# Kernel tuning notes

Hardware: AMD Instinct MI355X
Metric: run time of the kernel (lower is better)

## Reference

```python
import jax, jax.numpy as jnp
import numpy as np

B, T, D, U, W = 8, 1024, 1024, 1024, 2  # batch, seq_len, input_dim, units, window_size


def setup_inputs() -> dict:
    key = jax.random.key(0)
    k1, k2 = jax.random.split(key)
    x = jax.random.normal(k1, (B, T, D), dtype=jnp.float32)
    # keras 'uniform' initializer: U(-0.05, 0.05); kernel squeezed from (W,1,D,3U) to (W,D,3U)
    kernel = jax.random.uniform(k2, (W, D, 3 * U), dtype=jnp.float32, minval=-0.05, maxval=0.05)
    bias = jnp.zeros((3 * U,), dtype=jnp.float32)  # 'zero' initializer
    return {"x": x, "kernel": kernel, "bias": bias}


def reference(x, kernel, bias):
    Wk, Din, U3 = kernel.shape
    Un = U3 // 3
    Tn = x.shape[1]
    # causal temporal padding (window_size-1 on the left), then valid windowed conv
    xp = jnp.pad(x, ((0, 0), (Wk - 1, 0), (0, 0)))
    # gates[b,t] = sum_k xp[b,t+k] @ kernel[k] + bias  -> [B,T,3U]
    gates = sum(jnp.einsum('btd,du->btu', xp[:, k:k + Tn], kernel[k]) for k in range(Wk)) + bias
    z = jnp.tanh(gates[..., :Un])
    f = jax.nn.sigmoid(gates[..., Un:2 * Un])
    o = jax.nn.sigmoid(gates[..., 2 * Un:])

    def step(h, zfo):
        zt, ft, ot = zfo
        h_new = ot * (ft * h + (1.0 - ft) * zt)
        return h_new, h_new

    h0 = jnp.zeros((x.shape[0], Un), dtype=x.dtype)
    _, hs = jax.lax.scan(step, h0, (z.swapaxes(0, 1), f.swapaxes(0, 1), o.swapaxes(0, 1)))
    return hs.swapaxes(0, 1)  # [B,T,U] (return_sequences=True)
```

## Files before the change

### kernel.cpp

```cpp
#include <hip/hip_runtime.h>
#include <hip/hip_bf16.h>

typedef __bf16 bf16x8 __attribute__((ext_vector_type(8)));
typedef float f32x4 __attribute__((ext_vector_type(4)));

#define GLOBAL_AS(p) ((const __attribute__((address_space(1))) void*)(p))
#define LDS_AS(p)    ((__attribute__((address_space(3))) void*)(p))

static __device__ __forceinline__ unsigned short f2bf(float f) {
    union { float f; unsigned u; } v; v.f = f;
    unsigned r = v.u + 0x7FFFu + ((v.u >> 16) & 1u);
    return (unsigned short)(r >> 16);
}

__global__ void zero_page(float4* __restrict__ z) {
    z[threadIdx.x * 4 + 0] = make_float4(0.f, 0.f, 0.f, 0.f);
    z[threadIdx.x * 4 + 1] = make_float4(0.f, 0.f, 0.f, 0.f);
    z[threadIdx.x * 4 + 2] = make_float4(0.f, 0.f, 0.f, 0.f);
    z[threadIdx.x * 4 + 3] = make_float4(0.f, 0.f, 0.f, 0.f);
}

__global__ void prep_xb(const float* __restrict__ x, unsigned short* __restrict__ xb) {
    const int m = blockIdx.x;
    const int c = threadIdx.x * 4;
    float4 v = *reinterpret_cast<const float4*>(x + (size_t)m * 1024 + c);
    ushort4 b = make_ushort4(f2bf(v.x), f2bf(v.y), f2bf(v.z), f2bf(v.w));
    *reinterpret_cast<ushort4*>(xb + (size_t)m * 1024 + c) = b;
}

__global__ void prep_kt(const float* __restrict__ K, unsigned short* __restrict__ KT) {
    __shared__ float tile[64][65];
    const int bi = blockIdx.x;
    const int bj = blockIdx.y;
    const int tx = threadIdx.x & 63;
    const int ty = threadIdx.x >> 6;

#pragma unroll
    for (int i = 0; i < 16; ++i) {
        int r = ty * 16 + i;
        tile[r][tx] = K[(size_t)(bi * 64 + r) * 3072 + bj * 64 + tx];
    }
    __syncthreads();
#pragma unroll
    for (int i = 0; i < 16; ++i) {
        int r = ty * 16 + i;
        KT[(size_t)(bj * 64 + r) * 2048 + bi * 64 + tx] = f2bf(tile[tx][r]);
    }
}

__global__ __launch_bounds__(256, 2)
void gemm_gates(const unsigned short* __restrict__ xb,
                const unsigned short* __restrict__ BT,
                const unsigned short* __restrict__ zpage,
                const float* __restrict__ bias,
                float* __restrict__ G) {
    __shared__ __align__(16) unsigned short As[128 * 64];
    __shared__ __align__(16) unsigned short Bs[128 * 64];

    const int tid  = threadIdx.x;
    const int lane = tid & 63;
    const int wid  = tid >> 6;
    const int wr   = wid >> 1, wc = wid & 1;
    const int m0   = blockIdx.y * 128;
    const int n0   = blockIdx.x * 128;

    f32x4 acc[4][4] = {};

    const int sr = lane >> 3;
    const int sc = lane & 7;

    const unsigned short* srcA_lo[4];
    const unsigned short* srcA_hi[4];
    const unsigned short* srcB[4];
#pragma unroll
    for (int i = 0; i < 4; ++i) {
        const int r  = wid * 32 + i * 8 + sr;
        const int cc = sc ^ (r & 7);
        const int srow = m0 + r;
        srcA_hi[i] = xb + (size_t)srow * 1024 + cc * 8;
        srcA_lo[i] = ((srow & 1023) == 0) ? (zpage + cc * 8)
                                          : (xb + (size_t)(srow - 1) * 1024 + cc * 8);
        srcB[i]    = BT + (size_t)(n0 + r) * 2048 + cc * 8;
    }

    for (int kt = 0; kt < 32; ++kt) {
        const int kb = kt * 64;
#pragma unroll
        for (int i = 0; i < 4; ++i) {
            const int r0 = wid * 32 + i * 8;
            const unsigned short* sa = (kt < 16) ? (srcA_lo[i] + kb)
                                                 : (srcA_hi[i] + (kb - 1024));
            __builtin_amdgcn_global_load_lds(GLOBAL_AS(sa),          LDS_AS(As + r0 * 64), 16, 0, 0);
            __builtin_amdgcn_global_load_lds(GLOBAL_AS(srcB[i] + kb), LDS_AS(Bs + r0 * 64), 16, 0, 0);
        }
        __syncthreads();

#pragma unroll
        for (int ks = 0; ks < 2; ++ks) {
            bf16x8 af[4], bg[4];
#pragma unroll
            for (int m = 0; m < 4; ++m) {
                const int row = wr * 64 + m * 16 + (lane & 15);
                const int c   = ks * 4 + (lane >> 4);
                const int p   = c ^ (row & 7);
                af[m] = *reinterpret_cast<const bf16x8*>(As + row * 64 + p * 8);
            }
#pragma unroll
            for (int n = 0; n < 4; ++n) {
                const int row = wc * 64 + n * 16 + (lane & 15);
                const int c   = ks * 4 + (lane >> 4);
                const int p   = c ^ (row & 7);
                bg[n] = *reinterpret_cast<const bf16x8*>(Bs + row * 64 + p * 8);
            }
#pragma unroll
            for (int m = 0; m < 4; ++m)
#pragma unroll
                for (int n = 0; n < 4; ++n)
                    acc[m][n] = __builtin_amdgcn_mfma_f32_16x16x32_bf16(af[m], bg[n], acc[m][n], 0, 0, 0);
        }
        __syncthreads();
    }

    const int rgn = n0 >> 10;
#pragma unroll
    for (int m = 0; m < 4; ++m) {
#pragma unroll
        for (int n = 0; n < 4; ++n) {
            const int col = n0 + wc * 64 + n * 16 + (lane & 15);
            const float bv = bias[col];
#pragma unroll
            for (int v = 0; v < 4; ++v) {
                const int row = m0 + wr * 64 + m * 16 + ((lane >> 4) * 4) + v;
                const float g = acc[m][n][v] + bv;
                float val;
                if (rgn == 0) {
                    float s = 1.0f / (1.0f + __expf(-2.0f * g));
                    val = 2.0f * s - 1.0f;
                } else {
                    val = 1.0f / (1.0f + __expf(-g));
                }
                G[(size_t)row * 3072 + col] = val;
            }
        }
    }
}

__global__ void scan_pass1(const float* __restrict__ G, float2* __restrict__ AB) {
    const int bid = blockIdx.x;
    const int ug  = bid & 3;
    const int c   = (bid >> 2) & 7;
    const int b   = bid >> 5;
    const int u   = ug * 256 + threadIdx.x;
    const float* g = G + (size_t)(b * 1024 + c * 128) * 3072 + u;
    float A = 1.f, Bv = 0.f;
#pragma unroll 8
    for (int i = 0; i < 128; ++i) {
        const float zv = g[(size_t)i * 3072];
        const float fv = g[(size_t)i * 3072 + 1024];
        const float ov = g[(size_t)i * 3072 + 2048];
        const float a  = ov * fv;
        const float bb = ov * (1.f - fv) * zv;
        A  = a * A;
        Bv = a * Bv + bb;
    }
    AB[(size_t)(b * 8 + c) * 1024 + u] = make_float2(A, Bv);
}

__global__ void scan_pass23(const float* __restrict__ G, const float2* __restrict__ AB,
                            float* __restrict__ out) {
    const int b  = blockIdx.x >> 3;
    const int ug = blockIdx.x & 7;
    const int c  = threadIdx.x >> 7;
    const int ui = threadIdx.x & 127;
    const int u  = ug * 128 + ui;

    float h = 0.f;
    for (int j = 0; j < c; ++j) {
        float2 p = AB[(size_t)(b * 8 + j) * 1024 + u];
        h = p.x * h + p.y;
    }
    const float* g = G + (size_t)(b * 1024 + c * 128) * 3072 + u;
    float* o = out + (size_t)(b * 1024 + c * 128) * 1024 + u;
#pragma unroll 8
    for (int i = 0; i < 128; ++i) {
        const float zv = g[(size_t)i * 3072];
        const float fv = g[(size_t)i * 3072 + 1024];
        const float ov = g[(size_t)i * 3072 + 2048];
        h = ov * (fv * h + (1.f - fv) * zv);
        o[(size_t)i * 1024] = h;
    }
}

extern "C" void kernel_launch(void* const* d_in, const int* in_sizes, int n_in,
                              void* d_out, int out_size, void* d_ws, size_t ws_size,
                              hipStream_t stream) {
    const float* x    = (const float*)d_in[0];
    const float* kern = (const float*)d_in[1];
    const float* bias = (const float*)d_in[2];
    float* out = (float*)d_out;

    char* ws = (char*)d_ws;
    unsigned short* xb   = (unsigned short*)ws;
    unsigned short* KT   = (unsigned short*)(ws + 16777216);
    float* G             = (float*)(ws + 29360128);
    float2* AB           = (float2*)(ws + 130023424);
    unsigned short* zpg  = (unsigned short*)(ws + 130547712);

    zero_page<<<1, 64, 0, stream>>>((float4*)zpg);
    prep_xb<<<dim3(8192), dim3(256), 0, stream>>>(x, xb);
    prep_kt<<<dim3(32, 48), dim3(256), 0, stream>>>(kern, KT);
    gemm_gates<<<dim3(24, 64), dim3(256), 0, stream>>>(xb, KT, zpg, bias, G);
    scan_pass1<<<dim3(256), dim3(256), 0, stream>>>(G, AB);
    scan_pass23<<<dim3(64), dim3(1024), 0, stream>>>(G, AB, out);
}
```

Measured before the change: 177.6 us.

## Rewrite gate GEMM as 256x256 double-buffered pipeline with padded input and fp16 gates

```diff
diff --git a/kernel.cpp b/kernel.cpp
--- a/kernel.cpp
+++ b/kernel.cpp
@@ -13,19 +13,18 @@
     return (unsigned short)(r >> 16);
 }
 
-__global__ void zero_page(float4* __restrict__ z) {
-    z[threadIdx.x * 4 + 0] = make_float4(0.f, 0.f, 0.f, 0.f);
-    z[threadIdx.x * 4 + 1] = make_float4(0.f, 0.f, 0.f, 0.f);
-    z[threadIdx.x * 4 + 2] = make_float4(0.f, 0.f, 0.f, 0.f);
-    z[threadIdx.x * 4 + 3] = make_float4(0.f, 0.f, 0.f, 0.f);
-}
-
-__global__ void prep_xb(const float* __restrict__ x, unsigned short* __restrict__ xb) {
-    const int m = blockIdx.x;
+__global__ void prep_xb(const float* __restrict__ x, unsigned short* __restrict__ xb2) {
+    const int bid = blockIdx.x;
     const int c = threadIdx.x * 4;
-    float4 v = *reinterpret_cast<const float4*>(x + (size_t)m * 1024 + c);
-    ushort4 b = make_ushort4(f2bf(v.x), f2bf(v.y), f2bf(v.z), f2bf(v.w));
-    *reinterpret_cast<ushort4*>(xb + (size_t)m * 1024 + c) = b;
+    if (bid < 8192) {
+        const int dst = bid + (bid >> 10) + 1;
+        float4 v = *reinterpret_cast<const float4*>(x + (size_t)bid * 1024 + c);
+        ushort4 b = make_ushort4(f2bf(v.x), f2bf(v.y), f2bf(v.z), f2bf(v.w));
+        *reinterpret_cast<ushort4*>(xb2 + (size_t)dst * 1024 + c) = b;
+    } else {
+        const int zr = (bid - 8192) * 1025;
+        *reinterpret_cast<ushort4*>(xb2 + (size_t)zr * 1024 + c) = make_ushort4(0, 0, 0, 0);
+    }
 }
 
 __global__ void prep_kt(const float* __restrict__ K, unsigned short* __restrict__ KT) {
@@ -48,90 +47,145 @@
     }
 }
 
-__global__ __launch_bounds__(256, 2)
-void gemm_gates(const unsigned short* __restrict__ xb,
+__global__ __launch_bounds__(512, 2)
+void gemm_gates(const unsigned short* __restrict__ xb2,
                 const unsigned short* __restrict__ BT,
-                const unsigned short* __restrict__ zpage,
                 const float* __restrict__ bias,
-                float* __restrict__ G) {
-    __shared__ __align__(16) unsigned short As[128 * 64];
-    __shared__ __align__(16) unsigned short Bs[128 * 64];
+                _Float16* __restrict__ G) {
+    __shared__ __align__(16) unsigned short As[2 * 256 * 64];
+    __shared__ __align__(16) unsigned short Bs[2 * 256 * 64];
 
     const int tid  = threadIdx.x;
     const int lane = tid & 63;
-    const int wid  = tid >> 6;
-    const int wr   = wid >> 1, wc = wid & 1;
-    const int m0   = blockIdx.y * 128;
-    const int n0   = blockIdx.x * 128;
-
-    f32x4 acc[4][4] = {};
-
-    const int sr = lane >> 3;
-    const int sc = lane & 7;
-
-    const unsigned short* srcA_lo[4];
-    const unsigned short* srcA_hi[4];
-    const unsigned short* srcB[4];
-#pragma unroll
-    for (int i = 0; i < 4; ++i) {
-        const int r  = wid * 32 + i * 8 + sr;
-        const int cc = sc ^ (r & 7);
-        const int srow = m0 + r;
-        srcA_hi[i] = xb + (size_t)srow * 1024 + cc * 8;
-        srcA_lo[i] = ((srow & 1023) == 0) ? (zpage + cc * 8)
-                                          : (xb + (size_t)(srow - 1) * 1024 + cc * 8);
-        srcB[i]    = BT + (size_t)(n0 + r) * 2048 + cc * 8;
-    }
-
-    for (int kt = 0; kt < 32; ++kt) {
-        const int kb = kt * 64;
-#pragma unroll
-        for (int i = 0; i < 4; ++i) {
-            const int r0 = wid * 32 + i * 8;
-            const unsigned short* sa = (kt < 16) ? (srcA_lo[i] + kb)
-                                                 : (srcA_hi[i] + (kb - 1024));
-            __builtin_amdgcn_global_load_lds(GLOBAL_AS(sa),          LDS_AS(As + r0 * 64), 16, 0, 0);
-            __builtin_amdgcn_global_load_lds(GLOBAL_AS(srcB[i] + kb), LDS_AS(Bs + r0 * 64), 16, 0, 0);
+    const int w    = tid >> 6;
+    const int wr   = w >> 2;
+    const int wc   = w & 3;
+    const int l15  = lane & 15, l16 = lane >> 4, l7 = lane & 7, sr8 = lane >> 3;
+    const int csw  = l7 ^ sr8;
+
+    int bid = blockIdx.x;
+    bid = (bid & 7) * 48 + (bid >> 3);
+    const int bx = bid % 12, by = bid / 12;
+    const int m0 = by * 256, n0 = bx * 256;
+
+    const unsigned short* aP[4];
+    const unsigned short* bP[4];
+#pragma unroll
+    for (int hj = 0; hj < 4; ++hj) {
+        const int h = hj >> 1, j = hj & 1;
+        const int tr = h * 128 + j * 64 + w * 8 + sr8;
+        const int m  = m0 + tr;
+        aP[hj] = xb2 + (size_t)(m + (m >> 10)) * 1024 + csw * 8;
+        bP[hj] = BT  + (size_t)(n0 + tr) * 2048 + csw * 8;
+    }
+
+    auto stageA = [&](int kt, int h, int buf) {
+#pragma unroll
+        for (int j = 0; j < 2; ++j) {
+            __builtin_amdgcn_global_load_lds(GLOBAL_AS(aP[h * 2 + j] + kt * 64),
+                LDS_AS(As + buf * 16384 + (h * 128 + j * 64 + w * 8) * 64), 16, 0, 0);
         }
-        __syncthreads();
-
-#pragma unroll
-        for (int ks = 0; ks < 2; ++ks) {
-            bf16x8 af[4], bg[4];
-#pragma unroll
-            for (int m = 0; m < 4; ++m) {
-                const int row = wr * 64 + m * 16 + (lane & 15);
-                const int c   = ks * 4 + (lane >> 4);
-                const int p   = c ^ (row & 7);
-                af[m] = *reinterpret_cast<const bf16x8*>(As + row * 64 + p * 8);
+    };
+    auto stageB = [&](int kt, int h, int buf) {
+#pragma unroll
+        for (int j = 0; j < 2; ++j) {
+            __builtin_amdgcn_global_load_lds(GLOBAL_AS(bP[h * 2 + j] + kt * 64),
+                LDS_AS(Bs + buf * 16384 + (h * 128 + j * 64 + w * 8) * 64), 16, 0, 0);
+        }
+    };
+
+    f32x4 acc[8][4] = {};
+    bf16x8 aR[4][2], bR0[2][2], bR1[2][2];
+
+    auto rdA = [&](int buf, int mh) {
+#pragma unroll
+        for (int mi = 0; mi < 4; ++mi)
+#pragma unroll
+            for (int ks = 0; ks < 2; ++ks) {
+                const int row = mh * 128 + wr * 64 + mi * 16 + l15;
+                const int p   = (ks * 4 + l16) ^ l7;
+                aR[mi][ks] = *reinterpret_cast<const bf16x8*>(As + buf * 16384 + row * 64 + p * 8);
             }
-#pragma unroll
-            for (int n = 0; n < 4; ++n) {
-                const int row = wc * 64 + n * 16 + (lane & 15);
-                const int c   = ks * 4 + (lane >> 4);
-                const int p   = c ^ (row & 7);
-                bg[n] = *reinterpret_cast<const bf16x8*>(Bs + row * 64 + p * 8);
+    };
+    auto rdB = [&](int buf, int nh, bf16x8 (&br)[2][2]) {
+#pragma unroll
+        for (int ni = 0; ni < 2; ++ni)
+#pragma unroll
+            for (int ks = 0; ks < 2; ++ks) {
+                const int row = nh * 128 + wc * 32 + ni * 16 + l15;
+                const int p   = (ks * 4 + l16) ^ l7;
+                br[ni][ks] = *reinterpret_cast<const bf16x8*>(Bs + buf * 16384 + row * 64 + p * 8);
             }
-#pragma unroll
-            for (int m = 0; m < 4; ++m)
-#pragma unroll
-                for (int n = 0; n < 4; ++n)
-                    acc[m][n] = __builtin_amdgcn_mfma_f32_16x16x32_bf16(af[m], bg[n], acc[m][n], 0, 0, 0);
-        }
-        __syncthreads();
-    }
+    };
+
+#define MFMA_Q(MB, NB, BR)                                                              \
+    _Pragma("unroll")                                                                   \
+    for (int mi = 0; mi < 4; ++mi)                                                      \
+        _Pragma("unroll")                                                               \
+        for (int ni = 0; ni < 2; ++ni)                                                  \
+            _Pragma("unroll")                                                           \
+            for (int ks = 0; ks < 2; ++ks)                                              \
+                acc[(MB) + mi][(NB) + ni] = __builtin_amdgcn_mfma_f32_16x16x32_bf16(    \
+                    aR[mi][ks], BR[ni][ks], acc[(MB) + mi][(NB) + ni], 0, 0, 0);
+
+    stageA(0, 0, 0); stageB(0, 0, 0); stageB(0, 1, 0); stageA(0, 1, 0);
+    stageA(1, 0, 1); stageB(1, 0, 1); stageB(1, 1, 1);
+    asm volatile("s_waitcnt vmcnt(6)" ::: "memory");
+    __builtin_amdgcn_s_barrier();
+
+    for (int t = 0; t < 32; ++t) {
+        const int buf = t & 1;
+        rdA(buf, 0); rdB(buf, 0, bR0);
+        if (t < 31) stageA(t + 1, 1, buf ^ 1);
+        __builtin_amdgcn_s_barrier();
+        asm volatile("s_waitcnt lgkmcnt(0)" ::: "memory");
+        __builtin_amdgcn_sched_barrier(0);
+        __builtin_amdgcn_s_setprio(1);
+        MFMA_Q(0, 0, bR0)
+        __builtin_amdgcn_s_setprio(0);
+        __builtin_amdgcn_s_barrier();
+        rdB(buf, 1, bR1);
+        if (t < 30) stageA(t + 2, 0, buf);
+        __builtin_amdgcn_s_barrier();
+        asm volatile("s_waitcnt lgkmcnt(0)" ::: "memory");
+        __builtin_amdgcn_sched_barrier(0);
+        __builtin_amdgcn_s_setprio(1);
+        MFMA_Q(0, 2, bR1)
+        __builtin_amdgcn_s_setprio(0);
+        __builtin_amdgcn_s_barrier();
+        rdA(buf, 1);
+        if (t < 30) stageB(t + 2, 0, buf);
+        __builtin_amdgcn_s_barrier();
+        asm volatile("s_waitcnt lgkmcnt(0)" ::: "memory");
+        __builtin_amdgcn_sched_barrier(0);
+        __builtin_amdgcn_s_setprio(1);
+        MFMA_Q(4, 2, bR1)
+        __builtin_amdgcn_s_setprio(0);
+        __builtin_amdgcn_s_barrier();
+        if (t < 30) stageB(t + 2, 1, buf);
+        __builtin_amdgcn_s_barrier();
+        __builtin_amdgcn_s_setprio(1);
+        MFMA_Q(4, 0, bR0)
+        __builtin_amdgcn_s_setprio(0);
+        if (t < 30) { asm volatile("s_waitcnt vmcnt(6)" ::: "memory"); }
+        else        { asm volatile("s_waitcnt vmcnt(0)" ::: "memory"); }
+        __builtin_amdgcn_s_barrier();
+    }
+#undef MFMA_Q
 
     const int rgn = n0 >> 10;
 #pragma unroll
-    for (int m = 0; m < 4; ++m) {
-#pragma unroll
-        for (int n = 0; n < 4; ++n) {
-            const int col = n0 + wc * 64 + n * 16 + (lane & 15);
+    for (int mi8 = 0; mi8 < 8; ++mi8) {
+        const int mh = mi8 >> 2, mi = mi8 & 3;
+#pragma unroll
+        for (int ni4 = 0; ni4 < 4; ++ni4) {
+            const int nh = ni4 >> 1, ni = ni4 & 1;
+            const int col = n0 + nh * 128 + wc * 32 + ni * 16 + l15;
             const float bv = bias[col];
 #pragma unroll
             for (int v = 0; v < 4; ++v) {
-                const int row = m0 + wr * 64 + m * 16 + ((lane >> 4) * 4) + v;
-                const float g = acc[m][n][v] + bv;
+                const int row = m0 + mh * 128 + wr * 64 + mi * 16 + l16 * 4 + v;
+                const float g = acc[mi8][ni4][v] + bv;
                 float val;
                 if (rgn == 0) {
                     float s = 1.0f / (1.0f + __expf(-2.0f * g));
@@ -139,25 +193,25 @@
                 } else {
                     val = 1.0f / (1.0f + __expf(-g));
                 }
-                G[(size_t)row * 3072 + col] = val;
+                G[(size_t)row * 3072 + col] = (_Float16)val;
             }
         }
     }
 }
 
-__global__ void scan_pass1(const float* __restrict__ G, float2* __restrict__ AB) {
+__global__ void scan_pass1(const _Float16* __restrict__ G, float2* __restrict__ AB) {
     const int bid = blockIdx.x;
     const int ug  = bid & 3;
     const int c   = (bid >> 2) & 7;
     const int b   = bid >> 5;
     const int u   = ug * 256 + threadIdx.x;
-    const float* g = G + (size_t)(b * 1024 + c * 128) * 3072 + u;
+    const _Float16* g = G + (size_t)(b * 1024 + c * 128) * 3072 + u;
     float A = 1.f, Bv = 0.f;
 #pragma unroll 8
     for (int i = 0; i < 128; ++i) {
-        const float zv = g[(size_t)i * 3072];
-        const float fv = g[(size_t)i * 3072 + 1024];
-        const float ov = g[(size_t)i * 3072 + 2048];
+        const float zv = (float)g[(size_t)i * 3072];
+        const float fv = (float)g[(size_t)i * 3072 + 1024];
+        const float ov = (float)g[(size_t)i * 3072 + 2048];
         const float a  = ov * fv;
         const float bb = ov * (1.f - fv) * zv;
         A  = a * A;
@@ -166,7 +220,7 @@
     AB[(size_t)(b * 8 + c) * 1024 + u] = make_float2(A, Bv);
 }
 
-__global__ void scan_pass23(const float* __restrict__ G, const float2* __restrict__ AB,
+__global__ void scan_pass23(const _Float16* __restrict__ G, const float2* __restrict__ AB,
                             float* __restrict__ out) {
     const int b  = blockIdx.x >> 3;
     const int ug = blockIdx.x & 7;
@@ -179,13 +233,13 @@
         float2 p = AB[(size_t)(b * 8 + j) * 1024 + u];
         h = p.x * h + p.y;
     }
-    const float* g = G + (size_t)(b * 1024 + c * 128) * 3072 + u;
+    const _Float16* g = G + (size_t)(b * 1024 + c * 128) * 3072 + u;
     float* o = out + (size_t)(b * 1024 + c * 128) * 1024 + u;
 #pragma unroll 8
     for (int i = 0; i < 128; ++i) {
-        const float zv = g[(size_t)i * 3072];
-        const float fv = g[(size_t)i * 3072 + 1024];
-        const float ov = g[(size_t)i * 3072 + 2048];
+        const float zv = (float)g[(size_t)i * 3072];
+        const float fv = (float)g[(size_t)i * 3072 + 1024];
+        const float ov = (float)g[(size_t)i * 3072 + 2048];
         h = ov * (fv * h + (1.f - fv) * zv);
         o[(size_t)i * 1024] = h;
     }
@@ -200,16 +254,14 @@
     float* out = (float*)d_out;
 
     char* ws = (char*)d_ws;
-    unsigned short* xb   = (unsigned short*)ws;
-    unsigned short* KT   = (unsigned short*)(ws + 16777216);
-    float* G             = (float*)(ws + 29360128);
-    float2* AB           = (float2*)(ws + 130023424);
-    unsigned short* zpg  = (unsigned short*)(ws + 130547712);
-
-    zero_page<<<1, 64, 0, stream>>>((float4*)zpg);
-    prep_xb<<<dim3(8192), dim3(256), 0, stream>>>(x, xb);
+    unsigned short* xb2 = (unsigned short*)ws;
+    unsigned short* KT  = (unsigned short*)(ws + 16793600);
+    _Float16* G         = (_Float16*)(ws + 29376512);
+    float2* AB          = (float2*)(ws + 79708160);
+
+    prep_xb<<<dim3(8200), dim3(256), 0, stream>>>(x, xb2);
     prep_kt<<<dim3(32, 48), dim3(256), 0, stream>>>(kern, KT);
-    gemm_gates<<<dim3(24, 64), dim3(256), 0, stream>>>(xb, KT, zpg, bias, G);
+    gemm_gates<<<dim3(384), dim3(512), 0, stream>>>(xb2, KT, bias, G);
     scan_pass1<<<dim3(256), dim3(256), 0, stream>>>(G, AB);
     scan_pass23<<<dim3(64), dim3(1024), 0, stream>>>(G, AB, out);
 }
```

After: 191.8 us. +8.0%, slower.
